# Kernel optimization log

Measured on AMD Instinct MI355X. Metric: run time of the kernel, lower is better.

## Reference

```python
import jax, jax.numpy as jnp
import numpy as np

K = 5            # self.k
MARGIN_CB = 0.05  # neighborhood_ranking_crossbrain default margin
MARGIN_NRC = 0.4  # self.margin used in partial_nrc_loss
MAX_PAIRS = 6
EPS = 1e-8


def _norm(x):
    return x / jnp.sqrt(jnp.sum(x * x, axis=-1, keepdims=True) + 1e-12)


def _cos_dist_pair(a, b):
    s = jnp.clip(jnp.sum(a * b, axis=-1), -1.0 + EPS, 1.0 - EPS)
    return 1.0 - s


def _pairwise_cos_dist(x, y):
    return 1.0 - _norm(x) @ _norm(y).T


def _sq_dist(x):
    # squared euclidean distance -- same argsort order as torch.cdist
    sq = jnp.sum(x * x, axis=-1)
    return jnp.maximum(sq[:, None] + sq[None, :] - 2.0 * (x @ x.T), 0.0)


def _crossbrain(z1, z2, key):
    # neighborhood_ranking_crossbrain with match_idx = identity (as in forward)
    N = z1.shape[0]
    D1 = jax.lax.stop_gradient(_sq_dist(z1))      # ranking only, no grad
    neigh = jnp.argsort(D1, axis=-1)[:, 1:K + 1]  # (N, K) nearest neighbors
    # sample K distinct negatives per token excluding {n} U neigh[n]:
    scores = jax.random.uniform(key, (N, N))
    rows = jnp.arange(N)
    scores = scores.at[rows[:, None], neigh].set(-jnp.inf)
    scores = scores.at[rows, rows].set(-jnp.inf)
    _, neg = jax.lax.top_k(scores, K)             # (N, K)
    z2n = _norm(z2)
    anchor = z2n[:, None, :]                      # (N,1,C)
    d_pos = _cos_dist_pair(anchor, z2n[neigh])    # (N, K)
    d_neg = _cos_dist_pair(anchor, z2n[neg])      # (N, K)
    return jnp.mean(jax.nn.relu(d_pos - d_neg + MARGIN_CB))


def _nrc_partial(A, B, key):
    # partial_matches_mnn + nrc_on_partial, fully vectorized & masked
    T = A.shape[0]
    D = jax.lax.stop_gradient(_pairwise_cos_dist(A, B))
    b_of_a = jnp.argmin(D, axis=1)
    a_of_b = jnp.argmin(D, axis=0)
    ar = jnp.arange(T)
    mutual = ar == a_of_b[b_of_a]                 # matched A tokens (injective)
    idxB_of_A = jnp.where(mutual, b_of_a, -1)
    is_matched_B = (jnp.zeros(T, jnp.int32).at[b_of_a].add(mutual.astype(jnp.int32)) > 0)
    DA = jax.lax.stop_gradient(_pairwise_cos_dist(A, A))
    neigh = jnp.argsort(DA, axis=-1)[:, 1:K + 1]  # (T, K)
    DB = _pairwise_cos_dist(B, B)                 # grads flow through DB
    posB = idxB_of_A[neigh]                       # (T, K)
    pos_mask = posB >= 0
    # negative pool: unmatched B tokens (stable argsort puts False first)
    order = jnp.argsort(is_matched_B)
    neg_count = jnp.maximum(T - jnp.sum(is_matched_B.astype(jnp.int32)), 1)
    r = jax.random.randint(key, (T, K), 0, T)
    negB = order[r % neg_count]                   # sample with replacement
    uB = jnp.maximum(idxB_of_A, 0)[:, None]
    d_pos = DB[uB, jnp.maximum(posB, 0)]
    d_neg = DB[uB, negB]
    hinge = jax.nn.relu(d_pos - d_neg + MARGIN_NRC) * pos_mask
    per_tok = jnp.sum(hinge, axis=1) / jnp.maximum(jnp.sum(pos_mask, axis=1), 1)
    valid = mutual & jnp.any(pos_mask, axis=1)
    cnt = jnp.sum(valid.astype(jnp.float32))
    return jnp.where(cnt > 0, jnp.sum(per_tok * valid) / jnp.maximum(cnt, 1.0), 0.0)


def _partial_nrc_loss(z1, z2, key, seed):
    Bn = z1.shape[0]
    pairs = [(p, q) for p in range(Bn) for q in range(Bn) if p != q]
    rng = np.random.RandomState(seed)
    if len(pairs) > MAX_PAIRS:
        sel = rng.permutation(len(pairs))[:MAX_PAIRS]
        pairs = [pairs[i] for i in sel]
    ps = jnp.array([p for p, _ in pairs])
    qs = jnp.array([q for _, q in pairs])
    keys = jax.random.split(key, len(pairs))
    losses = jax.vmap(_nrc_partial)(z1[ps], z2[qs], keys)
    return jnp.mean(losses)


def _taco_loss(z1, z2):
    Bn = z1.shape[0]
    base = jax.random.key(42)
    k1, k2, k3, k4 = jax.random.split(base, 4)
    loss2 = (jnp.sum(jax.vmap(_crossbrain)(z1, z2, jax.random.split(k1, Bn)))
             + jnp.sum(jax.vmap(_crossbrain)(z2, z1, jax.random.split(k2, Bn)))) / Bn
    loss3 = _partial_nrc_loss(z1, z2, k3, 0) + _partial_nrc_loss(z2, z1, k4, 1)
    return 10.0 * loss2 + 10.0 * loss3


def setup_inputs() -> dict:
    key = jax.random.key(0)
    k1, k2 = jax.random.split(key)
    Bn, T, C = 4, 2048, 768
    z1 = jax.random.normal(k1, (Bn, T, C), dtype=jnp.float32)
    z2 = jax.random.normal(k2, (Bn, T, C), dtype=jnp.float32)
    return {"z1": z1, "z2": z2}


def reference(z1, z2):
    return _taco_loss(z1, z2)
```

## Files before the change

### kernel.cpp

```cpp
#include <hip/hip_runtime.h>
#include <cstdint>
#include <cstddef>

#define TT 2048
#define CC 768
#define KK 5
#define PCAP 64

typedef __attribute__((ext_vector_type(8))) short short8;
typedef __attribute__((ext_vector_type(4))) short short4v;
typedef __attribute__((ext_vector_type(4))) float float4v;

struct PairTab { int sa[12]; int sb[12]; };
struct PairMap { int src[12]; int tr[12]; };

#define N_SELF_BLK (8 * 136)
#define TP 132

__device__ __forceinline__ unsigned int mix_hash(unsigned int a, unsigned int b) {
  unsigned long long x = (((unsigned long long)a) << 32) | (unsigned long long)b;
  x ^= x >> 33; x *= 0xff51afd7ed558ccdULL;
  x ^= x >> 33; x *= 0xc4ceb9fe1a85ec53ULL;
  x ^= x >> 33;
  return (unsigned int)(x & 0xffffffffu);
}

__device__ __forceinline__ unsigned short f2bf(float x) {
  union { float f; unsigned int u; } v; v.f = x;
  unsigned int r = v.u + 0x7fffu + ((v.u >> 16) & 1u);
  return (unsigned short)(r >> 16);
}

__device__ __forceinline__ float bf2f(unsigned short u) {
  union { unsigned int i; float f; } v; v.i = ((unsigned int)u) << 16; return v.f;
}

__device__ __forceinline__ void gload_lds16(const void* g, void* l) {
  __builtin_amdgcn_global_load_lds(
      (const __attribute__((address_space(1))) unsigned int*)g,
      (__attribute__((address_space(3))) unsigned int*)l, 16, 0, 0);
}

__device__ __forceinline__ bool lexlt(float k1, int i1, float k2, int i2) {
  return k1 < k2 || (k1 == k2 && i1 < i2);
}

#define INS5(kk_, ii_, L)                                                        \
  if (lexlt(kk_, ii_, L##k[4], L##i[4])) {                                       \
    L##k[4] = kk_; L##i[4] = ii_;                                                \
    if (lexlt(L##k[4], L##i[4], L##k[3], L##i[3])) {                             \
      float tk = L##k[3]; int ti_ = L##i[3]; L##k[3] = L##k[4]; L##i[3] = L##i[4]; L##k[4] = tk; L##i[4] = ti_; \
      if (lexlt(L##k[3], L##i[3], L##k[2], L##i[2])) {                           \
        tk = L##k[2]; ti_ = L##i[2]; L##k[2] = L##k[3]; L##i[2] = L##i[3]; L##k[3] = tk; L##i[3] = ti_; \
        if (lexlt(L##k[2], L##i[2], L##k[1], L##i[1])) {                         \
          tk = L##k[1]; ti_ = L##i[1]; L##k[1] = L##k[2]; L##i[1] = L##i[2]; L##k[2] = tk; L##i[2] = ti_; \
          if (lexlt(L##k[1], L##i[1], L##k[0], L##i[0])) {                       \
            tk = L##k[0]; ti_ = L##i[0]; L##k[0] = L##k[1]; L##i[0] = L##i[1]; L##k[1] = tk; L##i[1] = ti_; \
          }                                                                      \
        }                                                                        \
      }                                                                          \
    }                                                                            \
  }

__global__ __launch_bounds__(192) void prep_kernel(const float* __restrict__ z1, const float* __restrict__ z2,
                                                   unsigned short* __restrict__ zb, float* __restrict__ sq,
                                                   float* __restrict__ inv) {
  int r = blockIdx.x;
  const float* p = (r < 4 * TT) ? (z1 + (size_t)r * CC) : (z2 + (size_t)(r - 4 * TT) * CC);
  unsigned short* o = zb + (size_t)r * CC;
  float4 v = ((const float4*)p)[threadIdx.x];
  float s = v.x * v.x + v.y * v.y + v.z * v.z + v.w * v.w;
  ushort4 u;
  u.x = f2bf(v.x); u.y = f2bf(v.y); u.z = f2bf(v.z); u.w = f2bf(v.w);
  ((ushort4*)o)[threadIdx.x] = u;
#pragma unroll
  for (int off = 32; off > 0; off >>= 1) s += __shfl_down(s, off, 64);
  __shared__ float wred[3];
  int lane = threadIdx.x & 63, w = threadIdx.x >> 6;
  if (lane == 0) wred[w] = s;
  __syncthreads();
  if (threadIdx.x == 0) {
    float tot = wred[0] + wred[1] + wred[2];
    sq[r] = tot; inv[r] = rsqrtf(tot + 1e-12f);
  }
}

struct SmemKL { unsigned short As[128 * 64]; unsigned short Bs[128 * 64]; };
union SmemU {
  SmemKL st;
  unsigned short tile[128 * TP];
};

__device__ __forceinline__ void gram_mainloop(const unsigned short* __restrict__ A,
                                              const unsigned short* __restrict__ B,
                                              int bm, int bn, SmemKL& st, float4v (&acc)[4][4]) {
  const int lane = threadIdx.x & 63, waveId = threadIdx.x >> 6;
  const int wm = (waveId >> 1) * 64, wn = (waveId & 1) * 64;
  const int lrow = lane & 15, lquad = lane >> 4;
  for (int kk = 0; kk < CC; kk += 64) {
#pragma unroll
    for (int c = 0; c < 4; ++c) {
      int l = c * 256 + threadIdx.x;
      int row = l >> 3, pc = l & 7;
      int sc = pc ^ (row & 7);
      gload_lds16(A + (size_t)(bm + row) * CC + kk + sc * 8, &st.As[l * 8]);
      gload_lds16(B + (size_t)(bn + row) * CC + kk + sc * 8, &st.Bs[l * 8]);
    }
    __syncthreads();
#pragma unroll
    for (int h = 0; h < 2; ++h) {
      short8 af[4], bfr[4];
#pragma unroll
      for (int i = 0; i < 4; ++i) {
        int ra = wm + i * 16 + lrow;
        int ca = (h * 4 + lquad) ^ (ra & 7);
        af[i] = *(const short8*)&st.As[ra * 64 + ca * 8];
        int rb = wn + i * 16 + lrow;
        int cb2 = (h * 4 + lquad) ^ (rb & 7);
        bfr[i] = *(const short8*)&st.Bs[rb * 64 + cb2 * 8];
      }
#pragma unroll
      for (int i = 0; i < 4; ++i)
#pragma unroll
        for (int j = 0; j < 4; ++j)
          acc[i][j] = __builtin_amdgcn_mfma_f32_16x16x32_bf16(af[i], bfr[j], acc[i][j], 0, 0, 0);
    }
    __syncthreads();
  }
}

__global__ __launch_bounds__(256, 4) void gram_self(const unsigned short* __restrict__ zb,
                                                    unsigned short* __restrict__ gram) {
  __shared__ SmemU sm;
  const int bid = blockIdx.x;
  int s = bid / 136;
  int t = bid % 136;
  int ti = 0;
  while (t >= 16 - ti) { t -= 16 - ti; ++ti; }
  int tj = ti + t;
  int bm = ti * 128, bn = tj * 128;
  const unsigned short* A = zb + (size_t)s * TT * CC;

  float4v acc[4][4];
#pragma unroll
  for (int i = 0; i < 4; ++i)
#pragma unroll
    for (int j = 0; j < 4; ++j) acc[i][j] = (float4v){0.f, 0.f, 0.f, 0.f};

  gram_mainloop(A, A, bm, bn, sm.st, acc);

  const int lane = threadIdx.x & 63, waveId = threadIdx.x >> 6;
  const int wm = (waveId >> 1) * 64, wn = (waveId & 1) * 64;
  const int lrow = lane & 15, lquad = lane >> 4;

#pragma unroll
  for (int i = 0; i < 4; ++i)
#pragma unroll
    for (int j = 0; j < 4; ++j)
#pragma unroll
      for (int r = 0; r < 4; ++r) {
        int lr = wm + i * 16 + lquad * 4 + r;
        int lc = wn + j * 16 + lrow;
        sm.tile[lr * TP + lc] = f2bf(acc[i][j][r]);
      }
  __syncthreads();
  unsigned short* G = gram + (size_t)s * TT * TT;
  for (int it = 0; it < 16; ++it) {
    int task = it * 256 + threadIdx.x;
    int r = task >> 5;
    int c = task & 31;
    short4v v = *(const short4v*)&sm.tile[r * TP + c * 4];
    *(short4v*)&G[(size_t)(bm + r) * TT + bn + c * 4] = v;
  }
  if (bm != bn) {
    for (int it = 0; it < 16; ++it) {
      int task = it * 256 + threadIdx.x;
      int cc = task >> 5;
      int q = task & 31;
      short4v v;
      v[0] = (short)sm.tile[(q * 4 + 0) * TP + cc];
      v[1] = (short)sm.tile[(q * 4 + 1) * TP + cc];
      v[2] = (short)sm.tile[(q * 4 + 2) * TP + cc];
      v[3] = (short)sm.tile[(q * 4 + 3) * TP + cc];
      *(short4v*)&G[(size_t)(bn + cc) * TT + bm + q * 4] = v;
    }
  }
}

__global__ __launch_bounds__(256, 4) void gram_cross(const unsigned short* __restrict__ zb,
                                                     const float* __restrict__ invAll, PairTab tab,
                                                     float* __restrict__ prow_v, int* __restrict__ prow_i,
                                                     float* __restrict__ pcol_v, int* __restrict__ pcol_i) {
  __shared__ SmemKL smk;
  __shared__ float sInvA[128], sInvB[128];
  __shared__ float rowv[2][128]; __shared__ int rowi[2][128];
  __shared__ float colv[2][128]; __shared__ int coli[2][128];

  const int cbid = blockIdx.x;
  const int p = cbid >> 8;
  const int tile = cbid & 255;
  const int bn = (tile & 15) * 128;
  const int bm = (tile >> 4) * 128;
  const unsigned short* A = zb + (size_t)tab.sa[p] * TT * CC;
  const unsigned short* B = zb + (size_t)tab.sb[p] * TT * CC;
  if (threadIdx.x < 128) sInvA[threadIdx.x] = invAll[(size_t)tab.sa[p] * TT + bm + threadIdx.x];
  else sInvB[threadIdx.x - 128] = invAll[(size_t)tab.sb[p] * TT + bn + threadIdx.x - 128];

  float4v acc[4][4];
#pragma unroll
  for (int i = 0; i < 4; ++i)
#pragma unroll
    for (int j = 0; j < 4; ++j) acc[i][j] = (float4v){0.f, 0.f, 0.f, 0.f};

  gram_mainloop(A, B, bm, bn, smk, acc);

  const int lane = threadIdx.x & 63, waveId = threadIdx.x >> 6;
  const int wm = (waveId >> 1) * 64, wn = (waveId & 1) * 64;
  const int lrow = lane & 15, lquad = lane >> 4;

  float rbv[4][4]; int rbi[4][4];
#pragma unroll
  for (int i = 0; i < 4; ++i)
#pragma unroll
    for (int r = 0; r < 4; ++r) { rbv[i][r] = INFINITY; rbi[i][r] = TT; }
#pragma unroll
  for (int i = 0; i < 4; ++i)
#pragma unroll
    for (int j = 0; j < 4; ++j) {
      int col = bn + wn + j * 16 + lrow;
      float ivb = sInvB[wn + j * 16 + lrow];
#pragma unroll
      for (int r = 0; r < 4; ++r) {
        float v = -acc[i][j][r] * ivb;
        if (v < rbv[i][r]) { rbv[i][r] = v; rbi[i][r] = col; }
      }
    }
#pragma unroll
  for (int m = 1; m <= 8; m <<= 1) {
#pragma unroll
    for (int i = 0; i < 4; ++i)
#pragma unroll
      for (int r = 0; r < 4; ++r) {
        float v2 = __shfl_xor(rbv[i][r], m, 64);
        int i2 = __shfl_xor(rbi[i][r], m, 64);
        if (v2 < rbv[i][r] || (v2 == rbv[i][r] && i2 < rbi[i][r])) { rbv[i][r] = v2; rbi[i][r] = i2; }
      }
  }
  if (lrow == 0) {
#pragma unroll
    for (int i = 0; i < 4; ++i)
#pragma unroll
      for (int r = 0; r < 4; ++r) {
        int lr = wm + i * 16 + lquad * 4 + r;
        rowv[wn >> 6][lr] = rbv[i][r]; rowi[wn >> 6][lr] = rbi[i][r];
      }
  }

  float cbv[4]; int cbi[4];
#pragma unroll
  for (int j = 0; j < 4; ++j) { cbv[j] = INFINITY; cbi[j] = TT; }
#pragma unroll
  for (int j = 0; j < 4; ++j)
#pragma unroll
    for (int i = 0; i < 4; ++i)
#pragma unroll
      for (int r = 0; r < 4; ++r) {
        int lr = wm + i * 16 + lquad * 4 + r;
        float v = -acc[i][j][r] * sInvA[lr];
        if (v < cbv[j]) { cbv[j] = v; cbi[j] = bm + lr; }
      }
#pragma unroll
  for (int m = 16; m <= 32; m <<= 1) {
#pragma unroll
    for (int j = 0; j < 4; ++j) {
      float v2 = __shfl_xor(cbv[j], m, 64);
      int i2 = __shfl_xor(cbi[j], m, 64);
      if (v2 < cbv[j] || (v2 == cbv[j] && i2 < cbi[j])) { cbv[j] = v2; cbi[j] = i2; }
    }
  }
  if (lquad == 0) {
#pragma unroll
    for (int j = 0; j < 4; ++j) {
      int lc = wn + j * 16 + lrow;
      colv[wm >> 6][lc] = cbv[j]; coli[wm >> 6][lc] = cbi[j];
    }
  }
  __syncthreads();

  int bj = bn >> 7, bi2 = bm >> 7;
  if (threadIdx.x < 128) {
    int t = threadIdx.x;
    float v0 = rowv[0][t], v1 = rowv[1][t];
    int i0 = rowi[0][t], i1 = rowi[1][t];
    bool take1 = (v1 < v0) || (v1 == v0 && i1 < i0);
    prow_v[((size_t)p * 16 + bj) * TT + bm + t] = take1 ? v1 : v0;
    prow_i[((size_t)p * 16 + bj) * TT + bm + t] = take1 ? i1 : i0;
  } else {
    int t = threadIdx.x - 128;
    float v0 = colv[0][t], v1 = colv[1][t];
    int i0 = coli[0][t], i1 = coli[1][t];
    bool take1 = (v1 < v0) || (v1 == v0 && i1 < i0);
    pcol_v[((size_t)p * 16 + bi2) * TT + bn + t] = take1 ? v1 : v0;
    pcol_i[((size_t)p * 16 + bi2) * TT + bn + t] = take1 ? i1 : i0;
  }
}

__device__ void top5_row_full(const unsigned short* __restrict__ G, const float* __restrict__ sq,
                              const float* __restrict__ inv, int i, int lane,
                              int* __restrict__ o0, int* __restrict__ o1) {
  float ak[5]; int ai[5];
  float bk[5]; int bi[5];
#pragma unroll
  for (int t = 0; t < 5; ++t) { ak[t] = INFINITY; ai[t] = TT; bk[t] = INFINITY; bi[t] = TT; }
#pragma unroll
  for (int step = 0; step < 8; ++step) {
    int j4 = (step * 64 + lane) * 4;
    ushort4 g4u = *(const ushort4*)&G[j4];
    float4 s4 = *(const float4*)&sq[j4];
    float4 v4 = *(const float4*)&inv[j4];
#pragma unroll
    for (int c = 0; c < 4; ++c) {
      int j = j4 + c;
      float g = bf2f((c == 0) ? g4u.x : (c == 1) ? g4u.y : (c == 2) ? g4u.z : g4u.w);
      float sv = (c == 0) ? s4.x : (c == 1) ? s4.y : (c == 2) ? s4.z : s4.w;
      float iv = (c == 0) ? v4.x : (c == 1) ? v4.y : (c == 2) ? v4.z : v4.w;
      float k0 = (j == i) ? INFINITY : sv - 2.f * g;
      float k1 = (j == i) ? INFINITY : -g * iv;
      INS5(k0, j, a)
      INS5(k1, j, b)
    }
  }
#pragma unroll
  for (int m = 1; m <= 32; m <<= 1) {
    float ok[5]; int oi[5];
#pragma unroll
    for (int t = 0; t < 5; ++t) { ok[t] = __shfl_xor(ak[t], m, 64); oi[t] = __shfl_xor(ai[t], m, 64); }
#pragma unroll
    for (int t = 0; t < 5; ++t) { INS5(ok[t], oi[t], a) }
#pragma unroll
    for (int t = 0; t < 5; ++t) { ok[t] = __shfl_xor(bk[t], m, 64); oi[t] = __shfl_xor(bi[t], m, 64); }
#pragma unroll
    for (int t = 0; t < 5; ++t) { INS5(ok[t], oi[t], b) }
  }
  if (lane < KK) {
    int v0 = (lane == 0) ? ai[0] : (lane == 1) ? ai[1] : (lane == 2) ? ai[2] : (lane == 3) ? ai[3] : ai[4];
    int v1 = (lane == 0) ? bi[0] : (lane == 1) ? bi[1] : (lane == 2) ? bi[2] : (lane == 3) ? bi[3] : bi[4];
    o0[lane] = v0;
    o1[lane] = v1;
  }
}

__global__ __launch_bounds__(256) void top5_batched(const unsigned short* __restrict__ gram,
                                                    const float* __restrict__ sqAll,
                                                    const float* __restrict__ invAll,
                                                    int* __restrict__ out0, int* __restrict__ out1) {
  int s = blockIdx.y;
  int w = threadIdx.x >> 6, lane = threadIdx.x & 63;
  int i = blockIdx.x * 4 + w;
  const unsigned short* G = gram + (size_t)s * TT * TT + (size_t)i * TT;
  const float* sq = sqAll + (size_t)s * TT;
  const float* inv = invAll + (size_t)s * TT;

  __shared__ float pvv[4][2][PCAP];
  __shared__ int pix[4][2][PCAP];
  __shared__ int pcnt[4][2];
  if (lane < 2) pcnt[w][lane] = 0;

  float mn0 = INFINITY, mn1 = INFINITY;
#pragma unroll
  for (int step = 0; step < 8; ++step) {
    int j4 = (step * 64 + lane) * 4;
    ushort4 g4u = *(const ushort4*)&G[j4];
    float4 s4 = *(const float4*)&sq[j4];
    float4 v4 = *(const float4*)&inv[j4];
#pragma unroll
    for (int c = 0; c < 4; ++c) {
      int j = j4 + c;
      float g = bf2f((c == 0) ? g4u.x : (c == 1) ? g4u.y : (c == 2) ? g4u.z : g4u.w);
      float sv = (c == 0) ? s4.x : (c == 1) ? s4.y : (c == 2) ? s4.z : s4.w;
      float iv = (c == 0) ? v4.x : (c == 1) ? v4.y : (c == 2) ? v4.z : v4.w;
      float k0 = (j == i) ? INFINITY : sv - 2.f * g;
      float k1 = (j == i) ? INFINITY : -g * iv;
      mn0 = fminf(mn0, k0);
      mn1 = fminf(mn1, k1);
    }
  }
#pragma unroll
  for (int m = 1; m <= 4; m <<= 1) {
    mn0 = fminf(mn0, __shfl_xor(mn0, m, 64));
    mn1 = fminf(mn1, __shfl_xor(mn1, m, 64));
  }
  float gv0[8], gv1[8];
#pragma unroll
  for (int g = 0; g < 8; ++g) {
    gv0[g] = __shfl(mn0, g * 8, 64);
    gv1[g] = __shfl(mn1, g * 8, 64);
  }
  float T0 = 0.f, T1 = 0.f;
#pragma unroll
  for (int g = 0; g < 8; ++g) {
    int r0 = 0, r1 = 0;
#pragma unroll
    for (int h = 0; h < 8; ++h) {
      r0 += ((gv0[h] < gv0[g]) || (gv0[h] == gv0[g] && h < g)) ? 1 : 0;
      r1 += ((gv1[h] < gv1[g]) || (gv1[h] == gv1[g] && h < g)) ? 1 : 0;
    }
    if (r0 == 4) T0 = gv0[g];
    if (r1 == 4) T1 = gv1[g];
  }

#pragma unroll
  for (int step = 0; step < 8; ++step) {
    int j4 = (step * 64 + lane) * 4;
    ushort4 g4u = *(const ushort4*)&G[j4];
    float4 s4 = *(const float4*)&sq[j4];
    float4 v4 = *(const float4*)&inv[j4];
#pragma unroll
    for (int c = 0; c < 4; ++c) {
      int j = j4 + c;
      float g = bf2f((c == 0) ? g4u.x : (c == 1) ? g4u.y : (c == 2) ? g4u.z : g4u.w);
      float sv = (c == 0) ? s4.x : (c == 1) ? s4.y : (c == 2) ? s4.z : s4.w;
      float iv = (c == 0) ? v4.x : (c == 1) ? v4.y : (c == 2) ? v4.z : v4.w;
      float k0 = (j == i) ? INFINITY : sv - 2.f * g;
      float k1 = (j == i) ? INFINITY : -g * iv;
      bool c0 = (k0 <= T0), c1 = (k1 <= T1);
      if (__any(c0)) {
        if (c0) {
          int q = atomicAdd(&pcnt[w][0], 1);
          if (q < PCAP) { pvv[w][0][q] = k0; pix[w][0][q] = j; }
        }
      }
      if (__any(c1)) {
        if (c1) {
          int q = atomicAdd(&pcnt[w][1], 1);
          if (q < PCAP) { pvv[w][1][q] = k1; pix[w][1][q] = j; }
        }
      }
    }
  }

  int c0n = pcnt[w][0], c1n = pcnt[w][1];
  if (c0n > PCAP || c1n > PCAP) {
    top5_row_full(G, sq, inv, i, lane,
                  out0 + ((size_t)s * TT + i) * KK, out1 + ((size_t)s * TT + i) * KK);
    return;
  }
  {
    float cv = (lane < c0n) ? pvv[w][0][lane] : INFINITY;
    int ci = (lane < c0n) ? pix[w][0][lane] : TT;
    int r = 0;
    for (int t = 0; t < c0n; ++t) {
      float ov = pvv[w][0][t]; int oi = pix[w][0][t];
      r += lexlt(ov, oi, cv, ci) ? 1 : 0;
    }
    if (lane < c0n && r < KK) out0[((size_t)s * TT + i) * KK + r] = ci;
  }
  {
    float cv = (lane < c1n) ? pvv[w][1][lane] : INFINITY;
    int ci = (lane < c1n) ? pix[w][1][lane] : TT;
    int r = 0;
    for (int t = 0; t < c1n; ++t) {
      float ov = pvv[w][1][t]; int oi = pix[w][1][t];
      r += lexlt(ov, oi, cv, ci) ? 1 : 0;
    }
    if (lane < c1n && r < KK) out1[((size_t)s * TT + i) * KK + r] = ci;
  }
}

__device__ void argmin_body(int bx, int p, const float* __restrict__ prow_v, const int* __restrict__ prow_i,
                            const float* __restrict__ pcol_v, const int* __restrict__ pcol_i,
                            const PairMap& pm,
                            int* __restrict__ b_of_a, int* __restrict__ a_of_b) {
  int u = pm.src[p];
  bool tr = pm.tr[p] != 0;
  int t = bx * 256 + threadIdx.x;
  int isRow = t < TT;
  int x = isRow ? t : t - TT;
  bool useRow = (isRow != 0) != tr;
  const float* pv = (useRow ? prow_v : pcol_v) + (size_t)u * 16 * TT;
  const int* pi = (useRow ? prow_i : pcol_i) + (size_t)u * 16 * TT;
  float best = INFINITY; int bidx = TT;
  for (int s = 0; s < 16; ++s) {
    float v = pv[(size_t)s * TT + x]; int id = pi[(size_t)s * TT + x];
    if (v < best || (v == best && id < bidx)) { best = v; bidx = id; }
  }
  if (isRow) b_of_a[(size_t)p * TT + x] = bidx;
  else       a_of_b[(size_t)p * TT + x] = bidx;
}

__device__ void cb_hinge_body(int bx, int c, const unsigned short* __restrict__ gram, const float* __restrict__ invAll,
                              const int* __restrict__ neigh1, float* __restrict__ cb_acc) {
  int i0 = bx * 64;
  int sa = c, sb = (c < 4) ? (c + 4) : (c - 4);
  const unsigned short* Gs = gram + (size_t)sb * TT * TT;
  const float* invB = invAll + (size_t)sb * TT;
  const int* neighA = neigh1 + (size_t)sa * TT * KK;
  unsigned int seed = 0x13579BDFu + 0x9E3779B9u * (unsigned)c;
  int tid = threadIdx.x;

  __shared__ int targ[64][10];
  __shared__ float sval[64][10];
  for (int t = tid; t < 64 * KK; t += 256) targ[t / KK][t % KK] = neighA[(size_t)i0 * KK + t];
  __syncthreads();
  if (tid < 64) {
    int i = i0 + tid;
    int pos[KK];
#pragma unroll
    for (int k = 0; k < KK; ++k) pos[k] = targ[tid][k];
    unsigned int ctr = 0;
    for (int k = 0; k < KK; ++k) {
      int cand;
      while (true) {
        unsigned int h = mix_hash(seed ^ (unsigned)i, ctr++);
        cand = (int)(h & (TT - 1));
        bool bad = (cand == i);
        for (int t = 0; t < KK; ++t) bad = bad || (cand == pos[t]);
        for (int t = 0; t < k; ++t) bad = bad || (cand == targ[tid][KK + t]);
        if (!bad) break;
      }
      targ[tid][KK + k] = cand;
    }
  }
  __syncthreads();
  for (int t = tid; t < 640; t += 256) {
    int il = t / 10, k = t % 10;
    int tt = targ[il][k];
    sval[il][k] = bf2f(Gs[(size_t)(i0 + il) * TT + tt]) * invB[tt];
  }
  __syncthreads();
  if (tid < 64) {
    int i = i0 + tid;
    float ii = invB[i];
    const float lo = -1.f + 1e-8f, hi = 1.f - 1e-8f;
    float hsum = 0.f;
#pragma unroll
    for (int k = 0; k < KK; ++k) {
      float sp = fminf(fmaxf(sval[tid][k] * ii, lo), hi);
      float sn = fminf(fmaxf(sval[tid][KK + k] * ii, lo), hi);
      float h = sn - sp + 0.05f;
      hsum += (h > 0.f) ? h : 0.f;
    }
#pragma unroll
    for (int off = 32; off > 0; off >>= 1) hsum += __shfl_down(hsum, off, 64);
    if (tid == 0) atomicAdd(&cb_acc[c], hsum);
  }
}

__global__ __launch_bounds__(256) void cb_argmin_fused(const unsigned short* __restrict__ gram,
                                                       const float* __restrict__ invAll,
                                                       const int* __restrict__ neigh1, float* __restrict__ cb_acc,
                                                       const float* __restrict__ prow_v, const int* __restrict__ prow_i,
                                                       const float* __restrict__ pcol_v, const int* __restrict__ pcol_i,
                                                       PairMap pm,
                                                       int* __restrict__ b_of_a, int* __restrict__ a_of_b) {
  unsigned int b = blockIdx.x;
  if (b < 256) {
    cb_hinge_body((int)(b & 31), (int)(b >> 5), gram, invAll, neigh1, cb_acc);
  } else {
    unsigned int t = b - 256;
    argmin_body((int)(t & 15), (int)(t >> 4), prow_v, prow_i, pcol_v, pcol_i, pm, b_of_a, a_of_b);
  }
}

__global__ __launch_bounds__(256) void mutual_batched(const int* __restrict__ b_of_a_all,
                                                      const int* __restrict__ a_of_b_all,
                                                      int* __restrict__ idxB_all, int* __restrict__ matchedB_all,
                                                      int* __restrict__ unmatched_all, int* __restrict__ scalars_all) {
  int p = blockIdx.x;
  const int* b_of_a = b_of_a_all + (size_t)p * TT;
  const int* a_of_b = a_of_b_all + (size_t)p * TT;
  int* idxB_of_A = idxB_all + (size_t)p * TT;
  int* matchedB = matchedB_all + (size_t)p * TT;
  int* unmatched = unmatched_all + (size_t)p * TT;
  __shared__ int cnt_sh;
  for (int j = threadIdx.x; j < TT; j += 256) matchedB[j] = 0;
  __syncthreads();
  for (int i = threadIdx.x; i < TT; i += 256) {
    int b = b_of_a[i];
    bool mut = (a_of_b[b] == i);
    idxB_of_A[i] = mut ? b : -1;
    if (mut) matchedB[b] = 1;
  }
  __syncthreads();
  if (threadIdx.x == 0) cnt_sh = 0;
  __syncthreads();
  for (int j = threadIdx.x; j < TT; j += 256) {
    if (!matchedB[j]) { int q = atomicAdd(&cnt_sh, 1); unmatched[q] = j; }
  }
  __syncthreads();
  if (threadIdx.x == 0) {
    int c = cnt_sh;
    if (c == 0) { unmatched[0] = 0; c = 1; }
    scalars_all[p * 16] = c;
  }
}

__global__ __launch_bounds__(256) void nrc_hinge_block(const unsigned short* __restrict__ gram, const float* __restrict__ invAll,
                                                       const int* __restrict__ neighC, const int* __restrict__ idxB_all,
                                                       const int* __restrict__ unmatched_all,
                                                       const int* __restrict__ scalars_all,
                                                       PairTab tab, float* __restrict__ nrc_acc) {
  int p = blockIdx.y;
  int i0 = blockIdx.x * 64;
  int sa = tab.sa[p], sb = tab.sb[p];
  const unsigned short* Gs = gram + (size_t)sb * TT * TT;
  const float* invB = invAll + (size_t)sb * TT;
  const int* neighA = neighC + (size_t)sa * TT * KK;
  const int* idxB_of_A = idxB_all + (size_t)p * TT;
  const int* unmatched = unmatched_all + (size_t)p * TT;
  unsigned int seed = 0xC0FFEE11u + 0x9E3779B9u * (unsigned)p;
  float* acc = nrc_acc + p * 2;
  int tid = threadIdx.x;

  __shared__ int targ[64][10];
  __shared__ float sval[64][10];
  __shared__ unsigned int tmask[64];
  __shared__ int su[64];
  if (tid < 64) { tmask[tid] = 0; su[tid] = idxB_of_A[i0 + tid]; }
  __syncthreads();
  unsigned int neg_count = (unsigned int)scalars_all[p * 16];
  for (int t = tid; t < 64 * KK; t += 256) {
    int il = t / KK, k = t % KK;
    int nb = neighA[(size_t)i0 * KK + t];
    int pb = idxB_of_A[nb];
    targ[il][k] = (pb >= 0) ? pb : 0;
    if (pb >= 0) atomicOr(&tmask[il], 1u << k);
  }
  for (int t = tid; t < 64 * KK; t += 256) {
    int il = t / KK, k = t % KK;
    int i = i0 + il;
    unsigned int r = mix_hash(seed ^ 0xA5A5u, (unsigned)(i * KK + k)) & (TT - 1);
    targ[il][KK + k] = unmatched[r % neg_count];
  }
  __syncthreads();
  for (int t = tid; t < 640; t += 256) {
    int il = t / 10, k = t % 10;
    int u = su[il] >= 0 ? su[il] : 0;
    int tt = targ[il][k];
    sval[il][k] = bf2f(Gs[(size_t)u * TT + tt]) * invB[tt];
  }
  __syncthreads();
  if (tid < 64) {
    int idx = su[tid];
    int u = idx >= 0 ? idx : 0;
    float iu = invB[u];
    unsigned int tm = tmask[tid];
    float hsum = 0.f; int pcnt = 0;
#pragma unroll
    for (int k = 0; k < KK; ++k) {
      if (tm & (1u << k)) {
        float dpos = 1.f - sval[tid][k] * iu;
        float dneg = 1.f - sval[tid][KK + k] * iu;
        float h = dpos - dneg + 0.4f;
        hsum += (h > 0.f) ? h : 0.f;
        pcnt++;
      }
    }
    float hs = 0.f, vc = 0.f;
    if (idx >= 0 && pcnt > 0) { hs = hsum / (float)pcnt; vc = 1.0f; }
#pragma unroll
    for (int off = 32; off > 0; off >>= 1) {
      hs += __shfl_down(hs, off, 64);
      vc += __shfl_down(vc, off, 64);
    }
    if (tid == 0) {
      atomicAdd(&acc[0], hs);
      atomicAdd(&acc[1], vc);
    }
  }
}

__global__ void final_kernel(const float* __restrict__ cb_acc, const float* __restrict__ nrc_acc,
                             float* __restrict__ out) {
  float loss2 = 0.f;
  for (int c = 0; c < 8; ++c) loss2 += cb_acc[c] * (1.0f / 10240.0f);
  loss2 *= 0.25f;
  float loss3 = 0.f;
  for (int d = 0; d < 2; ++d) {
    float s = 0.f;
    for (int t = 0; t < 6; ++t) {
      float cnt = nrc_acc[(d * 6 + t) * 2 + 1];
      float sum = nrc_acc[(d * 6 + t) * 2 + 0];
      s += (cnt > 0.f) ? (sum / cnt) : 0.f;
    }
    loss3 += s * (1.f / 6.f);
  }
  out[0] = 10.f * loss2 + 10.f * loss3;
}

namespace {
struct MT19937 {
  uint32_t mt[624]; int mti;
  void seed(uint32_t s) {
    mt[0] = s;
    for (int i = 1; i < 624; ++i) mt[i] = 1812433253u * (mt[i - 1] ^ (mt[i - 1] >> 30)) + (uint32_t)i;
    mti = 624;
  }
  uint32_t next() {
    if (mti >= 624) {
      for (int i = 0; i < 624; ++i) {
        uint32_t y = (mt[i] & 0x80000000u) | (mt[(i + 1) % 624] & 0x7fffffffu);
        uint32_t v = y >> 1;
        if (y & 1u) v ^= 0x9908b0dfu;
        mt[i] = mt[(i + 397) % 624] ^ v;
      }
      mti = 0;
    }
    uint32_t y = mt[mti++];
    y ^= y >> 11; y ^= (y << 7) & 0x9d2c5680u; y ^= (y << 15) & 0xefc60000u; y ^= y >> 18;
    return y;
  }
  uint32_t interval(uint32_t mx) {
    uint32_t mask = mx;
    mask |= mask >> 1; mask |= mask >> 2; mask |= mask >> 4; mask |= mask >> 8; mask |= mask >> 16;
    while (true) { uint32_t v = next() & mask; if (v <= mx) return v; }
  }
};
inline void np_perm12_first6(uint32_t seed, int* sel6) {
  int a[12]; for (int i = 0; i < 12; ++i) a[i] = i;
  MT19937 r; r.seed(seed);
  for (int i = 11; i >= 1; --i) { uint32_t j = r.interval((uint32_t)i); int t = a[i]; a[i] = a[j]; a[j] = t; }
  for (int i = 0; i < 6; ++i) sel6[i] = a[i];
}
}

extern "C" void kernel_launch(void* const* d_in, const int* in_sizes, int n_in,
                              void* d_out, int out_size, void* d_ws, size_t ws_size,
                              hipStream_t stream) {
  const float* z1 = (const float*)d_in[0];
  const float* z2 = (const float*)d_in[1];
  float* out = (float*)d_out;

  char* base = (char*)d_ws;
  size_t off = 0;
  auto alloc = [&](size_t bytes) -> void* {
    void* p = base + off;
    off = (off + bytes + 255) & ~(size_t)255;
    return p;
  };
  unsigned short* gram   = (unsigned short*)alloc((size_t)8 * TT * TT * 2);
  unsigned short* zb     = (unsigned short*)alloc((size_t)8 * TT * CC * 2);
  float* sq              = (float*)alloc((size_t)8 * TT * 4);
  float* inv             = (float*)alloc((size_t)8 * TT * 4);
  int*   neigh1          = (int*)alloc((size_t)8 * TT * KK * 4);
  int*   neighC          = (int*)alloc((size_t)8 * TT * KK * 4);
  float* prow_v          = (float*)alloc((size_t)12 * 16 * TT * 4);
  int*   prow_i          = (int*)alloc((size_t)12 * 16 * TT * 4);
  float* pcol_v          = (float*)alloc((size_t)12 * 16 * TT * 4);
  int*   pcol_i          = (int*)alloc((size_t)12 * 16 * TT * 4);
  int*   b_of_a          = (int*)alloc((size_t)12 * TT * 4);
  int*   a_of_b          = (int*)alloc((size_t)12 * TT * 4);
  int*   idxB            = (int*)alloc((size_t)12 * TT * 4);
  int*   matchedB        = (int*)alloc((size_t)12 * TT * 4);
  int*   unmatched       = (int*)alloc((size_t)12 * TT * 4);
  int*   scalars         = (int*)alloc(12 * 16 * 4);
  float* accs            = (float*)alloc(64 * 4);
  float* cb_acc          = accs;
  float* nrc_acc         = accs + 8;

  hipMemsetAsync(accs, 0, 64 * 4, stream);

  int sel0[6], sel1[6];
  np_perm12_first6(0u, sel0);
  np_perm12_first6(1u, sel1);
  static const int PP[12] = {0, 0, 0, 1, 1, 1, 2, 2, 2, 3, 3, 3};
  static const int QQ[12] = {1, 2, 3, 0, 2, 3, 0, 1, 3, 0, 1, 2};
  PairTab tab;
  for (int d = 0; d < 2; ++d) {
    const int* sel = (d == 0) ? sel0 : sel1;
    for (int t = 0; t < 6; ++t) {
      int pi_ = PP[sel[t]], qi = QQ[sel[t]];
      int p = d * 6 + t;
      tab.sa[p] = (d == 0) ? pi_ : 4 + pi_;
      tab.sb[p] = (d == 0) ? 4 + qi : qi;
    }
  }

  PairTab gtab; PairMap pm; int nU = 0;
  for (int p = 0; p < 12; ++p) {
    int f = -1, ftr = 0;
    for (int q = 0; q < nU; ++q) {
      if (gtab.sa[q] == tab.sb[p] && gtab.sb[q] == tab.sa[p]) { f = q; ftr = 1; break; }
      if (gtab.sa[q] == tab.sa[p] && gtab.sb[q] == tab.sb[p]) { f = q; ftr = 0; break; }
    }
    if (f >= 0) { pm.src[p] = f; pm.tr[p] = ftr; }
    else { gtab.sa[nU] = tab.sa[p]; gtab.sb[nU] = tab.sb[p]; pm.src[p] = nU; pm.tr[p] = 0; ++nU; }
  }

  prep_kernel<<<8 * TT, 192, 0, stream>>>(z1, z2, zb, sq, inv);

  gram_self<<<N_SELF_BLK, 256, 0, stream>>>(zb, gram);

  gram_cross<<<nU * 256, 256, 0, stream>>>(zb, inv, gtab, prow_v, prow_i, pcol_v, pcol_i);

  top5_batched<<<dim3(TT / 4, 8), 256, 0, stream>>>(gram, sq, inv, neigh1, neighC);

  cb_argmin_fused<<<256 + 192, 256, 0, stream>>>(gram, inv, neigh1, cb_acc,
                                                 prow_v, prow_i, pcol_v, pcol_i, pm, b_of_a, a_of_b);

  mutual_batched<<<12, 256, 0, stream>>>(b_of_a, a_of_b, idxB, matchedB, unmatched, scalars);
  nrc_hinge_block<<<dim3(TT / 64, 12), 256, 0, stream>>>(gram, inv, neighC, idxB, unmatched, scalars, tab, nrc_acc);

  final_kernel<<<1, 1, 0, stream>>>(cb_acc, nrc_acc, out);
}
```

Baseline: 314.1 us.

## Fuse tail kernels into cooperative kernel and precompute per-tile row minima in gram epilogue

Moves the per-row minimum computation for top-5 thresholding into the gram_self epilogue, writing per-128-column-tile minima that top5 then ranks with 16-lane shuffles instead of rescanning the gram row. Replaces the top5, cb/argmin, mutual, nrc and final launches with one cooperative kernel that uses grid syncs between phases. The accumulator memset is folded into prep_kernel. This removes launch gaps and a pass over the gram rows, but adds serial per-thread loops to the gram epilogue and grid-sync overhead, and the cooperative grid size is limited by occupancy.

```diff
diff --git a/kernel.cpp b/kernel.cpp
--- a/kernel.cpp
+++ b/kernel.cpp
@@ -1,6 +1,9 @@
 #include <hip/hip_runtime.h>
+#include <hip/hip_cooperative_groups.h>
 #include <cstdint>
 #include <cstddef>
+
+namespace cg = cooperative_groups;
 
 #define TT 2048
 #define CC 768
@@ -64,8 +67,9 @@
 
 __global__ __launch_bounds__(192) void prep_kernel(const float* __restrict__ z1, const float* __restrict__ z2,
                                                    unsigned short* __restrict__ zb, float* __restrict__ sq,
-                                                   float* __restrict__ inv) {
+                                                   float* __restrict__ inv, float* __restrict__ accs) {
   int r = blockIdx.x;
+  if (r == 0 && threadIdx.x < 64) accs[threadIdx.x] = 0.f;
   const float* p = (r < 4 * TT) ? (z1 + (size_t)r * CC) : (z2 + (size_t)(r - 4 * TT) * CC);
   unsigned short* o = zb + (size_t)r * CC;
   float4 v = ((const float4*)p)[threadIdx.x];
@@ -130,8 +134,12 @@
 }
 
 __global__ __launch_bounds__(256, 4) void gram_self(const unsigned short* __restrict__ zb,
-                                                    unsigned short* __restrict__ gram) {
+                                                    unsigned short* __restrict__ gram,
+                                                    const float* __restrict__ sqAll,
+                                                    const float* __restrict__ invAll,
+                                                    float* __restrict__ pmin0, float* __restrict__ pmin1) {
   __shared__ SmemU sm;
+  __shared__ float sqN[128], invN[128], sqM[128], invM[128];
   const int bid = blockIdx.x;
   int s = bid / 136;
   int t = bid % 136;
@@ -140,6 +148,10 @@
   int tj = ti + t;
   int bm = ti * 128, bn = tj * 128;
   const unsigned short* A = zb + (size_t)s * TT * CC;
+  const float* sqS = sqAll + (size_t)s * TT;
+  const float* invS = invAll + (size_t)s * TT;
+  if (threadIdx.x < 128) { sqN[threadIdx.x] = sqS[bn + threadIdx.x]; invN[threadIdx.x] = invS[bn + threadIdx.x]; }
+  else { sqM[threadIdx.x - 128] = sqS[bm + threadIdx.x - 128]; invM[threadIdx.x - 128] = invS[bm + threadIdx.x - 128]; }
 
   float4v acc[4][4];
 #pragma unroll
@@ -184,6 +196,28 @@
       v[3] = (short)sm.tile[(q * 4 + 3) * TP + cc];
       *(short4v*)&G[(size_t)(bn + cc) * TT + bm + q * 4] = v;
     }
+  }
+  if (threadIdx.x < 128) {
+    int r = threadIdx.x;
+    float m0 = INFINITY, m1 = INFINITY;
+    for (int c = 0; c < 128; ++c) {
+      if (bm == bn && c == r) continue;
+      float g = bf2f(sm.tile[r * TP + c]);
+      m0 = fminf(m0, sqN[c] - 2.f * g);
+      m1 = fminf(m1, -g * invN[c]);
+    }
+    pmin0[((size_t)s * 16 + (bn >> 7)) * TT + bm + r] = m0;
+    pmin1[((size_t)s * 16 + (bn >> 7)) * TT + bm + r] = m1;
+  } else if (bm != bn) {
+    int c = threadIdx.x - 128;
+    float m0 = INFINITY, m1 = INFINITY;
+    for (int r = 0; r < 128; ++r) {
+      float g = bf2f(sm.tile[r * TP + c]);
+      m0 = fminf(m0, sqM[r] - 2.f * g);
+      m1 = fminf(m1, -g * invM[r]);
+    }
+    pmin0[((size_t)s * 16 + (bm >> 7)) * TT + bn + c] = m0;
+    pmin1[((size_t)s * 16 + (bm >> 7)) * TT + bn + c] = m1;
   }
 }
 
@@ -350,13 +384,12 @@
   }
 }
 
-__global__ __launch_bounds__(256) void top5_batched(const unsigned short* __restrict__ gram,
-                                                    const float* __restrict__ sqAll,
-                                                    const float* __restrict__ invAll,
-                                                    int* __restrict__ out0, int* __restrict__ out1) {
-  int s = blockIdx.y;
+__device__ void top5_body(int s, int bx, const unsigned short* __restrict__ gram,
+                          const float* __restrict__ sqAll, const float* __restrict__ invAll,
+                          const float* __restrict__ pmin0, const float* __restrict__ pmin1,
+                          int* __restrict__ out0, int* __restrict__ out1) {
   int w = threadIdx.x >> 6, lane = threadIdx.x & 63;
-  int i = blockIdx.x * 4 + w;
+  int i = bx * 4 + w;
   const unsigned short* G = gram + (size_t)s * TT * TT + (size_t)i * TT;
   const float* sq = sqAll + (size_t)s * TT;
   const float* inv = invAll + (size_t)s * TT;
@@ -366,48 +399,23 @@
   __shared__ int pcnt[4][2];
   if (lane < 2) pcnt[w][lane] = 0;
 
-  float mn0 = INFINITY, mn1 = INFINITY;
-#pragma unroll
-  for (int step = 0; step < 8; ++step) {
-    int j4 = (step * 64 + lane) * 4;
-    ushort4 g4u = *(const ushort4*)&G[j4];
-    float4 s4 = *(const float4*)&sq[j4];
-    float4 v4 = *(const float4*)&inv[j4];
-#pragma unroll
-    for (int c = 0; c < 4; ++c) {
-      int j = j4 + c;
-      float g = bf2f((c == 0) ? g4u.x : (c == 1) ? g4u.y : (c == 2) ? g4u.z : g4u.w);
-      float sv = (c == 0) ? s4.x : (c == 1) ? s4.y : (c == 2) ? s4.z : s4.w;
-      float iv = (c == 0) ? v4.x : (c == 1) ? v4.y : (c == 2) ? v4.z : v4.w;
-      float k0 = (j == i) ? INFINITY : sv - 2.f * g;
-      float k1 = (j == i) ? INFINITY : -g * iv;
-      mn0 = fminf(mn0, k0);
-      mn1 = fminf(mn1, k1);
-    }
-  }
-#pragma unroll
-  for (int m = 1; m <= 4; m <<= 1) {
-    mn0 = fminf(mn0, __shfl_xor(mn0, m, 64));
-    mn1 = fminf(mn1, __shfl_xor(mn1, m, 64));
-  }
-  float gv0[8], gv1[8];
-#pragma unroll
-  for (int g = 0; g < 8; ++g) {
-    gv0[g] = __shfl(mn0, g * 8, 64);
-    gv1[g] = __shfl(mn1, g * 8, 64);
-  }
-  float T0 = 0.f, T1 = 0.f;
-#pragma unroll
-  for (int g = 0; g < 8; ++g) {
-    int r0 = 0, r1 = 0;
-#pragma unroll
-    for (int h = 0; h < 8; ++h) {
-      r0 += ((gv0[h] < gv0[g]) || (gv0[h] == gv0[g] && h < g)) ? 1 : 0;
-      r1 += ((gv1[h] < gv1[g]) || (gv1[h] == gv1[g] && h < g)) ? 1 : 0;
-    }
-    if (r0 == 4) T0 = gv0[g];
-    if (r1 == 4) T1 = gv1[g];
-  }
+  int t16 = lane & 15;
+  float m0 = pmin0[((size_t)s * 16 + t16) * TT + i];
+  float m1 = pmin1[((size_t)s * 16 + t16) * TT + i];
+  int r0 = 0, r1 = 0;
+#pragma unroll
+  for (int d = 1; d < 16; ++d) {
+    int h = (t16 + d) & 15;
+    int src = (lane & 48) | h;
+    float o0 = __shfl(m0, src, 64);
+    float o1 = __shfl(m1, src, 64);
+    r0 += (o0 < m0 || (o0 == m0 && h < t16)) ? 1 : 0;
+    r1 += (o1 < m1 || (o1 == m1 && h < t16)) ? 1 : 0;
+  }
+  unsigned long long b0 = __ballot(r0 == 4);
+  unsigned long long b1 = __ballot(r1 == 4);
+  float T0 = __shfl(m0, (int)(__ffsll(b0) - 1), 64);
+  float T1 = __shfl(m1, (int)(__ffsll(b1) - 1), 64);
 
 #pragma unroll
   for (int step = 0; step < 8; ++step) {
@@ -440,30 +448,30 @@
   }
 
   int c0n = pcnt[w][0], c1n = pcnt[w][1];
-  if (c0n > PCAP || c1n > PCAP) {
+  if (c0n > PCAP || c1n > PCAP || c0n < KK || c1n < KK) {
     top5_row_full(G, sq, inv, i, lane,
                   out0 + ((size_t)s * TT + i) * KK, out1 + ((size_t)s * TT + i) * KK);
-    return;
-  }
-  {
-    float cv = (lane < c0n) ? pvv[w][0][lane] : INFINITY;
-    int ci = (lane < c0n) ? pix[w][0][lane] : TT;
-    int r = 0;
-    for (int t = 0; t < c0n; ++t) {
-      float ov = pvv[w][0][t]; int oi = pix[w][0][t];
-      r += lexlt(ov, oi, cv, ci) ? 1 : 0;
-    }
-    if (lane < c0n && r < KK) out0[((size_t)s * TT + i) * KK + r] = ci;
-  }
-  {
-    float cv = (lane < c1n) ? pvv[w][1][lane] : INFINITY;
-    int ci = (lane < c1n) ? pix[w][1][lane] : TT;
-    int r = 0;
-    for (int t = 0; t < c1n; ++t) {
-      float ov = pvv[w][1][t]; int oi = pix[w][1][t];
-      r += lexlt(ov, oi, cv, ci) ? 1 : 0;
-    }
-    if (lane < c1n && r < KK) out1[((size_t)s * TT + i) * KK + r] = ci;
+  } else {
+    {
+      float cv = (lane < c0n) ? pvv[w][0][lane] : INFINITY;
+      int ci = (lane < c0n) ? pix[w][0][lane] : TT;
+      int r = 0;
+      for (int t = 0; t < c0n; ++t) {
+        float ov = pvv[w][0][t]; int oi = pix[w][0][t];
+        r += lexlt(ov, oi, cv, ci) ? 1 : 0;
+      }
+      if (lane < c0n && r < KK) out0[((size_t)s * TT + i) * KK + r] = ci;
+    }
+    {
+      float cv = (lane < c1n) ? pvv[w][1][lane] : INFINITY;
+      int ci = (lane < c1n) ? pix[w][1][lane] : TT;
+      int r = 0;
+      for (int t = 0; t < c1n; ++t) {
+        float ov = pvv[w][1][t]; int oi = pix[w][1][t];
+        r += lexlt(ov, oi, cv, ci) ? 1 : 0;
+      }
+      if (lane < c1n && r < KK) out1[((size_t)s * TT + i) * KK + r] = ci;
+    }
   }
 }
 
@@ -546,27 +554,10 @@
   }
 }
 
-__global__ __launch_bounds__(256) void cb_argmin_fused(const unsigned short* __restrict__ gram,
-                                                       const float* __restrict__ invAll,
-                                                       const int* __restrict__ neigh1, float* __restrict__ cb_acc,
-                                                       const float* __restrict__ prow_v, const int* __restrict__ prow_i,
-                                                       const float* __restrict__ pcol_v, const int* __restrict__ pcol_i,
-                                                       PairMap pm,
-                                                       int* __restrict__ b_of_a, int* __restrict__ a_of_b) {
-  unsigned int b = blockIdx.x;
-  if (b < 256) {
-    cb_hinge_body((int)(b & 31), (int)(b >> 5), gram, invAll, neigh1, cb_acc);
-  } else {
-    unsigned int t = b - 256;
-    argmin_body((int)(t & 15), (int)(t >> 4), prow_v, prow_i, pcol_v, pcol_i, pm, b_of_a, a_of_b);
-  }
-}
-
-__global__ __launch_bounds__(256) void mutual_batched(const int* __restrict__ b_of_a_all,
-                                                      const int* __restrict__ a_of_b_all,
-                                                      int* __restrict__ idxB_all, int* __restrict__ matchedB_all,
-                                                      int* __restrict__ unmatched_all, int* __restrict__ scalars_all) {
-  int p = blockIdx.x;
+__device__ void mutual_body(int p, const int* __restrict__ b_of_a_all,
+                            const int* __restrict__ a_of_b_all,
+                            int* __restrict__ idxB_all, int* __restrict__ matchedB_all,
+                            int* __restrict__ unmatched_all, int* __restrict__ scalars_all) {
   const int* b_of_a = b_of_a_all + (size_t)p * TT;
   const int* a_of_b = a_of_b_all + (size_t)p * TT;
   int* idxB_of_A = idxB_all + (size_t)p * TT;
@@ -595,13 +586,11 @@
   }
 }
 
-__global__ __launch_bounds__(256) void nrc_hinge_block(const unsigned short* __restrict__ gram, const float* __restrict__ invAll,
-                                                       const int* __restrict__ neighC, const int* __restrict__ idxB_all,
-                                                       const int* __restrict__ unmatched_all,
-                                                       const int* __restrict__ scalars_all,
-                                                       PairTab tab, float* __restrict__ nrc_acc) {
-  int p = blockIdx.y;
-  int i0 = blockIdx.x * 64;
+__device__ void nrc_body(int bx, int p, const unsigned short* __restrict__ gram, const float* __restrict__ invAll,
+                         const int* __restrict__ neighC, const int* __restrict__ idxB_all,
+                         const int* __restrict__ unmatched_all, const int* __restrict__ scalars_all,
+                         const PairTab& tab, float* __restrict__ nrc_acc) {
+  int i0 = bx * 64;
   int sa = tab.sa[p], sb = tab.sb[p];
   const unsigned short* Gs = gram + (size_t)sb * TT * TT;
   const float* invB = invAll + (size_t)sb * TT;
@@ -670,22 +659,61 @@
   }
 }
 
-__global__ void final_kernel(const float* __restrict__ cb_acc, const float* __restrict__ nrc_acc,
-                             float* __restrict__ out) {
-  float loss2 = 0.f;
-  for (int c = 0; c < 8; ++c) loss2 += cb_acc[c] * (1.0f / 10240.0f);
-  loss2 *= 0.25f;
-  float loss3 = 0.f;
-  for (int d = 0; d < 2; ++d) {
-    float s = 0.f;
-    for (int t = 0; t < 6; ++t) {
-      float cnt = nrc_acc[(d * 6 + t) * 2 + 1];
-      float sum = nrc_acc[(d * 6 + t) * 2 + 0];
-      s += (cnt > 0.f) ? (sum / cnt) : 0.f;
-    }
-    loss3 += s * (1.f / 6.f);
-  }
-  out[0] = 10.f * loss2 + 10.f * loss3;
+__global__ __launch_bounds__(256) void tail_coop(const unsigned short* __restrict__ gram,
+                                                 const float* __restrict__ sqAll,
+                                                 const float* __restrict__ invAll,
+                                                 const float* __restrict__ pmin0,
+                                                 const float* __restrict__ pmin1,
+                                                 int* __restrict__ neigh1, int* __restrict__ neighC,
+                                                 const float* __restrict__ prow_v, const int* __restrict__ prow_i,
+                                                 const float* __restrict__ pcol_v, const int* __restrict__ pcol_i,
+                                                 PairMap pm, int* __restrict__ b_of_a, int* __restrict__ a_of_b,
+                                                 float* __restrict__ cb_acc,
+                                                 int* __restrict__ idxB, int* __restrict__ matchedB,
+                                                 int* __restrict__ unmatched, int* __restrict__ scalars,
+                                                 PairTab tab, float* __restrict__ nrc_acc,
+                                                 float* __restrict__ out) {
+  cg::grid_group grid = cg::this_grid();
+
+  for (unsigned int u = blockIdx.x; u < 4288u; u += gridDim.x) {
+    if (u < 4096u) top5_body((int)(u >> 9), (int)(u & 511), gram, sqAll, invAll, pmin0, pmin1, neigh1, neighC);
+    else {
+      unsigned int t = u - 4096u;
+      argmin_body((int)(t & 15), (int)(t >> 4), prow_v, prow_i, pcol_v, pcol_i, pm, b_of_a, a_of_b);
+    }
+    __syncthreads();
+  }
+  grid.sync();
+
+  for (unsigned int u = blockIdx.x; u < 268u; u += gridDim.x) {
+    if (u < 256u) cb_hinge_body((int)(u & 31), (int)(u >> 5), gram, invAll, neigh1, cb_acc);
+    else mutual_body((int)(u - 256u), b_of_a, a_of_b, idxB, matchedB, unmatched, scalars);
+    __syncthreads();
+  }
+  grid.sync();
+
+  for (unsigned int u = blockIdx.x; u < 384u; u += gridDim.x) {
+    nrc_body((int)(u & 31), (int)(u >> 5), gram, invAll, neighC, idxB, unmatched, scalars, tab, nrc_acc);
+    __syncthreads();
+  }
+  grid.sync();
+
+  if (blockIdx.x == 0 && threadIdx.x == 0) {
+    float loss2 = 0.f;
+    for (int c = 0; c < 8; ++c) loss2 += cb_acc[c] * (1.0f / 10240.0f);
+    loss2 *= 0.25f;
+    float loss3 = 0.f;
+    for (int d = 0; d < 2; ++d) {
+      float s = 0.f;
+      for (int t = 0; t < 6; ++t) {
+        float cnt = nrc_acc[(d * 6 + t) * 2 + 1];
+        float sum = nrc_acc[(d * 6 + t) * 2 + 0];
+        s += (cnt > 0.f) ? (sum / cnt) : 0.f;
+      }
+      loss3 += s * (1.f / 6.f);
+    }
+    out[0] = 10.f * loss2 + 10.f * loss3;
+  }
 }
 
 namespace {
@@ -744,6 +772,8 @@
   float* inv             = (float*)alloc((size_t)8 * TT * 4);
   int*   neigh1          = (int*)alloc((size_t)8 * TT * KK * 4);
   int*   neighC          = (int*)alloc((size_t)8 * TT * KK * 4);
+  float* pmin0           = (float*)alloc((size_t)8 * 16 * TT * 4);
+  float* pmin1           = (float*)alloc((size_t)8 * 16 * TT * 4);
   float* prow_v          = (float*)alloc((size_t)12 * 16 * TT * 4);
   int*   prow_i          = (int*)alloc((size_t)12 * 16 * TT * 4);
   float* pcol_v          = (float*)alloc((size_t)12 * 16 * TT * 4);
@@ -758,8 +788,6 @@
   float* cb_acc          = accs;
   float* nrc_acc         = accs + 8;
 
-  hipMemsetAsync(accs, 0, 64 * 4, stream);
-
   int sel0[6], sel1[6];
   np_perm12_first6(0u, sel0);
   np_perm12_first6(1u, sel1);
@@ -787,19 +815,26 @@
     else { gtab.sa[nU] = tab.sa[p]; gtab.sb[nU] = tab.sb[p]; pm.src[p] = nU; pm.tr[p] = 0; ++nU; }
   }
 
-  prep_kernel<<<8 * TT, 192, 0, stream>>>(z1, z2, zb, sq, inv);
-
-  gram_self<<<N_SELF_BLK, 256, 0, stream>>>(zb, gram);
+  static int coop_grid = 0;
+  if (coop_grid == 0) {
+    int maxb = 0;
+    hipError_t e = hipOccupancyMaxActiveBlocksPerMultiprocessor(&maxb, tail_coop, 256, 0);
+    if (e != hipSuccess || maxb < 1) maxb = 1;
+    coop_grid = maxb * 256;
+    if (coop_grid > 4288) coop_grid = 4288;
+  }
+
+  prep_kernel<<<8 * TT, 192, 0, stream>>>(z1, z2, zb, sq, inv, accs);
+
+  gram_self<<<N_SELF_BLK, 256, 0, stream>>>(zb, gram, sq, inv, pmin0, pmin1);
 
   gram_cross<<<nU * 256, 256, 0, stream>>>(zb, inv, gtab, prow_v, prow_i, pcol_v, pcol_i);
 
-  top5_batched<<<dim3(TT / 4, 8), 256, 0, stream>>>(gram, sq, inv, neigh1, neighC);
-
-  cb_argmin_fused<<<256 + 192, 256, 0, stream>>>(gram, inv, neigh1, cb_acc,
-                                                 prow_v, prow_i, pcol_v, pcol_i, pm, b_of_a, a_of_b);
-
-  mutual_batched<<<12, 256, 0, stream>>>(b_of_a, a_of_b, idxB, matchedB, unmatched, scalars);
-  nrc_hinge_block<<<dim3(TT / 64, 12), 256, 0, stream>>>(gram, inv, neighC, idxB, unmatched, scalars, tab, nrc_acc);
-
-  final_kernel<<<1, 1, 0, stream>>>(cb_acc, nrc_acc, out);
-}
+  void* args[] = {(void*)&gram, (void*)&sq, (void*)&inv, (void*)&pmin0, (void*)&pmin1,
+                  (void*)&neigh1, (void*)&neighC,
+                  (void*)&prow_v, (void*)&prow_i, (void*)&pcol_v, (void*)&pcol_i,
+                  (void*)&pm, (void*)&b_of_a, (void*)&a_of_b,
+                  (void*)&cb_acc, (void*)&idxB, (void*)&matchedB, (void*)&unmatched, (void*)&scalars,
+                  (void*)&tab, (void*)&nrc_acc, (void*)&out};
+  hipLaunchCooperativeKernel((void*)tail_coop, dim3(coop_grid), dim3(256), args, 0, stream);
+}
```

New measurement: 488.0 us. +55.4%, slower.
